# Kernel optimization log

Measured on AMD Instinct MI355X. Metric: run time of the kernel, lower is better.

## Reference

```python
import jax, jax.numpy as jnp
import numpy as np

WINDOW_SHAPE = (11, 11, 11)
CHANNELS = 1


def gaussian_nd(shape, sigma=1.0, mu=0.0):
    # n-dimensional gaussian kernel, identical to the torch source
    m = np.meshgrid(*[np.linspace(-1, 1, s) for s in shape])
    d = np.sqrt(np.sum([x * x for x in m], axis=0))
    g = np.exp(-((d - mu) ** 2 / (2.0 * sigma ** 2)))
    return g / np.sum(g)


def setup_inputs() -> dict:
    key = jax.random.key(0)
    k1, k2 = jax.random.split(key)
    shape = (2, 1, 96, 256, 256)  # N, C, D, H, W
    img1 = jax.random.uniform(k1, shape, dtype=jnp.float32)
    img2 = jax.random.uniform(k2, shape, dtype=jnp.float32)
    # depthwise window, shape (C, 1, 11, 11, 11) == (O, I/groups, D, H, W)
    w = jnp.asarray(gaussian_nd(WINDOW_SHAPE), dtype=jnp.float32)
    window = jnp.broadcast_to(w[None, None], (CHANNELS, 1) + WINDOW_SHAPE)
    return {"img1": img1, "img2": img2, "window": window}


def _blur(x, window):
    # depthwise 3D conv, padding=0 (VALID), groups=CHANNELS
    return jax.lax.conv_general_dilated(
        x, window, window_strides=(1, 1, 1), padding="VALID",
        dimension_numbers=("NCDHW", "OIDHW", "NCDHW"),
        feature_group_count=CHANNELS)


def reference(img1, img2, window):
    mu1 = _blur(img1, window)
    mu2 = _blur(img2, window)
    mu1_sq = mu1 * mu1
    mu2_sq = mu2 * mu2
    mu1_mu2 = mu1 * mu2
    sigma1_sq = _blur(img1 * img1, window) - mu1_sq
    sigma2_sq = _blur(img2 * img2, window) - mu2_sq
    sigma12 = _blur(img1 * img2, window) - mu1_mu2
    C1 = 0.01 ** 2
    C2 = 0.03 ** 2
    ssim_map = ((2 * mu1_mu2 + C1) * (2 * sigma12 + C2)
                / ((mu1_sq + mu2_sq + C1) * (sigma1_sq + sigma2_sq + C2)))
    # size_average=True -> scalar mean
    return jnp.mean(ssim_map)
```

## Files before the change

kernel.cpp:

```cpp
#include <hip/hip_runtime.h>
#include <hip/hip_fp16.h>

#define KW 11
#define NB 2
#define DI 96
#define HI 256
#define WI 256
#define DOUT 86
#define HOUT 246
#define WOUT 246
#define HT 16
#define WT 16
#define DCH 3
#define RR 26
#define HSZ (HI * WI)
#define SSIM_C1 1e-4f
#define SSIM_C2 9e-4f
#define NBLK (16 * 16 * NB * DCH)
#define RAW1_SLOT 364
#define RAW_SLOT 728

typedef const unsigned int __attribute__((address_space(1)))* gp1_t;
typedef unsigned int __attribute__((address_space(3)))* lp3_t;
using f32x2 = __attribute__((ext_vector_type(2))) float;
using f32x4 = __attribute__((ext_vector_type(4))) float;

__device__ __forceinline__ void gl_lds16(const float* g, float* l) {
    __builtin_amdgcn_global_load_lds((gp1_t)(const void*)g, (lp3_t)(void*)l, 16, 0, 0);
}

__device__ __forceinline__ f32x2 pk_fma_s(f32x2 w, f32x2 x, f32x2 acc) {
    f32x2 d;
    asm("v_pk_fma_f32 %0, %1, %2, %3" : "=v"(d) : "s"(w), "v"(x), "v"(acc));
    return d;
}

__device__ __forceinline__ unsigned pk_fma_h(unsigned w, unsigned x, unsigned acc) {
    unsigned d;
    asm("v_pk_fma_f16 %0, %1, %2, %3" : "=v"(d) : "s"(w), "v"(x), "v"(acc));
    return d;
}

__device__ __forceinline__ unsigned pkrtz(float a, float b) {
    auto h = __builtin_amdgcn_cvt_pkrtz(a, b);
    return __builtin_bit_cast(unsigned, h);
}

__device__ __forceinline__ f32x2 h2f(unsigned u) {
    f32x2 r;
    r.x = __half2float(__ushort_as_half((unsigned short)(u & 0xffffu)));
    r.y = __half2float(__ushort_as_half((unsigned short)(u >> 16)));
    return r;
}

__device__ __forceinline__ float rfl(float x) {
    return __int_as_float(__builtin_amdgcn_readfirstlane(__float_as_int(x)));
}

template<int J>
__device__ __forceinline__ void acc_step_h(
    unsigned (&AB)[KW], unsigned (&PQ)[KW], const unsigned (&wh)[KW],
    unsigned f12, unsigned f34, bool emit, unsigned& o12, unsigned& o34)
{
    #pragma unroll
    for (int p = 0; p < KW; ++p) {
        const int s = (J - p + KW) % KW;
        AB[s] = pk_fma_h(wh[p], f12, AB[s]);
        PQ[s] = pk_fma_h(wh[p], f34, PQ[s]);
    }
    const int C = (J + 1) % KW;
    if (emit) { o12 = AB[C]; o34 = PQ[C]; }
    AB[C] = 0u;
    PQ[C] = 0u;
}

static __global__ __launch_bounds__(256, 2) void ssim_main(
    const float* __restrict__ img1, const float* __restrict__ img2,
    const float* __restrict__ win, float* __restrict__ bsum)
{
    __shared__ __align__(16) float rawf[RAW_SLOT * 4];
    __shared__ __align__(16) uint2 a4h[RR][17][2];
    float* const tmpw = (float*)a4h;
    float* const w1s  = (float*)a4h + 128;
    float* const red  = (float*)a4h + 140;

    const int t = threadIdx.x;
    const int bz = blockIdx.z;
    const int n = (bz >= DCH) ? 1 : 0;
    const int chunk = bz - n * DCH;
    const int d0 = (chunk == 0) ? 0 : (chunk == 1 ? 30 : 58);
    const int dpc = (chunk == 0) ? 30 : 28;
    const int NIT = (dpc + KW - 1) >> 1;
    const int h0 = blockIdx.y * HT, w0 = blockIdx.x * WT;

    if (t < 121) {
        const int i = t / KW, j = t - i * KW;
        const float* wp = win + i * (KW * KW) + j * KW;
        float s = 0.f;
        #pragma unroll
        for (int m = 0; m < KW; ++m) s += wp[m];
        tmpw[t] = s;
    }
    __syncthreads();
    if (t < KW) {
        float s = 0.f;
        #pragma unroll
        for (int j = 0; j < KW; ++j) s += tmpw[t * KW + j];
        w1s[t] = s;
    }
    __syncthreads();
    f32x2 w2[KW];
    unsigned whq[KW];
    #pragma unroll
    for (int k = 0; k < KW; ++k) {
        const float ws = rfl(w1s[k]);
        w2[k] = (f32x2){ws, ws};
        const unsigned hb = (unsigned)__half_as_ushort(__float2half(ws));
        whq[k] = __builtin_amdgcn_readfirstlane(hb | (hb << 16));
    }
    __syncthreads();

    unsigned soff[2];
    #pragma unroll
    for (int q = 0; q < 2; ++q) {
        const int s = t + 256 * q;
        const int sl = (s >= 182) ? 1 : 0;
        const int v = (s < RAW1_SLOT ? s : 0) - sl * 182;
        const int r = v / 7;
        const int c = v - 7 * r;
        const int gh = h0 + r, gw0 = w0 + 4 * c;
        const bool oob = (s >= RAW1_SLOT) || (gh >= HI) || (gw0 >= WI);
        soff[q] = oob ? 0u
                      : (unsigned)((((n * DI + d0 + sl) * HSZ) + gh * WI + gw0) * 4);
    }
    #define STAGE() do { \
        gl_lds16((const float*)((const char*)img1 + soff[0]), &rawf[4 * t]); \
        gl_lds16((const float*)((const char*)img2 + soff[0]), &rawf[RAW1_SLOT * 4 + 4 * t]); \
        if (t < RAW1_SLOT - 256) { \
            gl_lds16((const float*)((const char*)img1 + soff[1]), &rawf[1024 + 4 * t]); \
            gl_lds16((const float*)((const char*)img2 + soff[1]), &rawf[RAW1_SLOT * 4 + 1024 + 4 * t]); \
        } \
        soff[0] += 8 * HSZ; soff[1] += 8 * HSZ; \
    } while (0)

    unsigned rABh[KW], rPQh[KW];
    #pragma unroll
    for (int p = 0; p < KW; ++p) { rABh[p] = 0u; rPQh[p] = 0u; }

    const int ty = t >> 4, tx = t & 15;
    const bool valid = (h0 + ty < HOUT) && (w0 + tx < WOUT);
    float partial = 0.f;

    const int paSl = (t >= 104) ? 1 : 0;
    const int paV  = (t < 208 ? t : 0) - paSl * 104;
    const int paCg = paV / 26;
    const int paR  = paV - paCg * 26;
    const float* const paA = &rawf[(paSl * 182 + paR * 7) * 4];
    const float* const paB = paA + RAW1_SLOT * 4;
    uint2* const paW = &a4h[paR][4 * paCg][paSl];

    auto phaseA = [&]() {
        f32x2 s12[4] = {{0.f,0.f},{0.f,0.f},{0.f,0.f},{0.f,0.f}};
        f32x2 s34[4] = {{0.f,0.f},{0.f,0.f},{0.f,0.f},{0.f,0.f}};
        #pragma unroll
        for (int q = 0; q < 4; ++q) {
            const f32x4 aq = *(const f32x4*)(paA + 4 * (paCg + q));
            const f32x4 bq = *(const f32x4*)(paB + 4 * (paCg + q));
            #pragma unroll
            for (int j = 0; j < 4; ++j) {
                const int m = 4 * q + j;
                if (m < 14) {
                    f32x2 pxy = (f32x2){aq[j], bq[j]};
                    pxy += (f32x2){-0.5f, -0.5f};
                    const float x = pxy.x, y = pxy.y;
                    const f32x2 pts = (f32x2){x * y, fmaf(x, x, y * y)};
                    #pragma unroll
                    for (int o = 0; o < 4; ++o) {
                        const int k = m - o;
                        if (k >= 0 && k <= 10) {
                            s12[o] = pk_fma_s(w2[k], pxy, s12[o]);
                            s34[o] = pk_fma_s(w2[k], pts, s34[o]);
                        }
                    }
                }
            }
        }
        #pragma unroll
        for (int o = 0; o < 4; ++o)
            paW[2 * o] = make_uint2(pkrtz(s12[o].x, s12[o].y),
                                    pkrtz(s34[o].x, s34[o].y));
    };

    STAGE();
    __syncthreads();

    int jj = 0;
    for (int i = 0; i < NIT; ++i) {
        if (t < 208) phaseA();
        __syncthreads();

        if (i + 1 < NIT) STAGE();

        unsigned ha12 = 0u, ha34 = 0u, hb12 = 0u, hb34 = 0u;
        #pragma unroll
        for (int kh = 0; kh < KW; ++kh) {
            const uint4 v = *(const uint4*)&a4h[ty + kh][tx][0];
            ha12 = pk_fma_h(whq[kh], v.x, ha12);
            ha34 = pk_fma_h(whq[kh], v.y, ha34);
            hb12 = pk_fma_h(whq[kh], v.z, hb12);
            hb34 = pk_fma_h(whq[kh], v.w, hb34);
        }

        const bool emit = (i >= 5);
        unsigned oa12u = 0u, oa34u = 0u, ob12u = 0u, ob34u = 0u;
        switch (jj) {
            #define CASE2(J) case J: \
                acc_step_h<J>(rABh, rPQh, whq, ha12, ha34, emit, oa12u, oa34u); \
                acc_step_h<(J+1)%KW>(rABh, rPQh, whq, hb12, hb34, emit, ob12u, ob34u); \
                break;
            CASE2(0) CASE2(1) CASE2(2) CASE2(3) CASE2(4) CASE2(5)
            CASE2(6) CASE2(7) CASE2(8) CASE2(9) CASE2(10)
            #undef CASE2
        }
        jj += 2; if (jj >= KW) jj -= KW;

        if (emit && valid) {
            {
                const f32x2 v12 = h2f(oa12u), v34 = h2f(oa34u);
                const float a = v12.x, b = v12.y;
                const float mu1 = a + 0.5f, mu2 = b + 0.5f;
                const float m11 = mu1 * mu1, m22 = mu2 * mu2, m12 = mu1 * mu2;
                const float s12c = v34.x - a * b;
                const float ssum = v34.y - a * a - b * b;
                const float num = (2.f * m12 + SSIM_C1) * (2.f * s12c + SSIM_C2);
                const float den = (m11 + m22 + SSIM_C1) * (ssum + SSIM_C2);
                partial += num * __builtin_amdgcn_rcpf(den);
            }
            {
                const f32x2 v12 = h2f(ob12u), v34 = h2f(ob34u);
                const float a = v12.x, b = v12.y;
                const float mu1 = a + 0.5f, mu2 = b + 0.5f;
                const float m11 = mu1 * mu1, m22 = mu2 * mu2, m12 = mu1 * mu2;
                const float s12c = v34.x - a * b;
                const float ssum = v34.y - a * a - b * b;
                const float num = (2.f * m12 + SSIM_C1) * (2.f * s12c + SSIM_C2);
                const float den = (m11 + m22 + SSIM_C1) * (ssum + SSIM_C2);
                partial += num * __builtin_amdgcn_rcpf(den);
            }
        }
        __syncthreads();
    }

    #pragma unroll
    for (int off = 32; off >= 1; off >>= 1)
        partial += __shfl_down(partial, off, 64);
    if ((t & 63) == 0) red[t >> 6] = partial;
    __syncthreads();
    if (t == 0) {
        bsum[(blockIdx.z * gridDim.y + blockIdx.y) * gridDim.x + blockIdx.x]
            = red[0] + red[1] + red[2] + red[3];
    }
}

static __global__ __launch_bounds__(256) void ssim_reduce(
    const float* __restrict__ bsum, float* __restrict__ out)
{
    __shared__ double red[4];
    const int t = threadIdx.x;
    double s = 0.0;
    for (int i = t; i < NBLK; i += 256) s += (double)bsum[i];
    #pragma unroll
    for (int off = 32; off >= 1; off >>= 1)
        s += __shfl_down(s, off, 64);
    if ((t & 63) == 0) red[t >> 6] = s;
    __syncthreads();
    if (t == 0) {
        const double tot = red[0] + red[1] + red[2] + red[3];
        out[0] = (float)(tot / (double)((long)NB * DOUT * HOUT * WOUT));
    }
}

extern "C" void kernel_launch(void* const* d_in, const int* in_sizes, int n_in,
                              void* d_out, int out_size, void* d_ws, size_t ws_size,
                              hipStream_t stream)
{
    const float* img1 = (const float*)d_in[0];
    const float* img2 = (const float*)d_in[1];
    const float* win  = (const float*)d_in[2];
    float* out  = (float*)d_out;
    float* bsum = (float*)d_ws;

    dim3 grid(16, 16, NB * DCH);
    ssim_main<<<grid, 256, 0, stream>>>(img1, img2, win, bsum);
    ssim_reduce<<<1, 256, 0, stream>>>(bsum, out);
}
```

Before: 90.28 us.

## Widen tiles to 32 columns with 512-thread blocks and four depth chunks

Doubles the output tile width to 32 and block size to 512 threads. The depth split becomes four uniform chunks of 22 slices instead of three uneven ones. The staging layout interleaves img1 and img2 per row, uses pointer strides with three load slots per thread, and expands the phase-A and reduction indexing. This cuts the horizontal halo overhead per output (the 10-column halo is spread over 32 rather than 16 columns) and changes the grid shape. In exchange, shared memory and register pressure per block grow, which may lower occupancy.

```diff
diff --git a/kernel.cpp b/kernel.cpp
--- a/kernel.cpp
+++ b/kernel.cpp
@@ -10,15 +10,18 @@
 #define HOUT 246
 #define WOUT 246
 #define HT 16
-#define WT 16
-#define DCH 3
+#define WT 32
+#define DCH 4
+#define DPC 22
 #define RR 26
 #define HSZ (HI * WI)
 #define SSIM_C1 1e-4f
 #define SSIM_C2 9e-4f
-#define NBLK (16 * 16 * NB * DCH)
-#define RAW1_SLOT 364
-#define RAW_SLOT 728
+#define NBLK (8 * 16 * NB * DCH)
+#define ROW_SLOT 23
+#define SLICE_SLOT (RR * ROW_SLOT)
+#define PAIR_SLOT (2 * SLICE_SLOT)
+#define NSTG 3
 
 typedef const unsigned int __attribute__((address_space(1)))* gp1_t;
 typedef unsigned int __attribute__((address_space(3)))* lp3_t;
@@ -74,22 +77,21 @@
     PQ[C] = 0u;
 }
 
-static __global__ __launch_bounds__(256, 2) void ssim_main(
+static __global__ __launch_bounds__(512, 2) void ssim_main(
     const float* __restrict__ img1, const float* __restrict__ img2,
     const float* __restrict__ win, float* __restrict__ bsum)
 {
-    __shared__ __align__(16) float rawf[RAW_SLOT * 4];
-    __shared__ __align__(16) uint2 a4h[RR][17][2];
+    __shared__ __align__(16) float rawf[PAIR_SLOT * 4];
+    __shared__ __align__(16) uint2 a4h[RR][33][2];
     float* const tmpw = (float*)a4h;
     float* const w1s  = (float*)a4h + 128;
-    float* const red  = (float*)a4h + 140;
+    float* const red  = (float*)a4h + 144;
 
     const int t = threadIdx.x;
     const int bz = blockIdx.z;
-    const int n = (bz >= DCH) ? 1 : 0;
-    const int chunk = bz - n * DCH;
-    const int d0 = (chunk == 0) ? 0 : (chunk == 1 ? 30 : 58);
-    const int dpc = (chunk == 0) ? 30 : 28;
+    const int n = bz >> 2, chunk = bz & 3;
+    const int d0 = chunk * DPC;
+    const int dpc = (DOUT - d0 < DPC) ? (DOUT - d0) : DPC;
     const int NIT = (dpc + KW - 1) >> 1;
     const int h0 = blockIdx.y * HT, w0 = blockIdx.x * WT;
 
@@ -120,43 +122,45 @@
     }
     __syncthreads();
 
-    unsigned soff[2];
-    #pragma unroll
-    for (int q = 0; q < 2; ++q) {
-        const int s = t + 256 * q;
-        const int sl = (s >= 182) ? 1 : 0;
-        const int v = (s < RAW1_SLOT ? s : 0) - sl * 182;
-        const int r = v / 7;
-        const int c = v - 7 * r;
+    const float* tp[NSTG];
+    int tstr[NSTG];
+    #pragma unroll
+    for (int q = 0; q < NSTG; ++q) {
+        const int u = t + 512 * q;
+        const int sl = (u >= SLICE_SLOT) ? 1 : 0;
+        const int v = (u < PAIR_SLOT ? u : 0) - sl * SLICE_SLOT;
+        const int r = v / ROW_SLOT;
+        const int rem = v - r * ROW_SLOT;
+        const int img = (rem >= 11) ? 1 : 0;
+        const int c = rem - 11 * img;
         const int gh = h0 + r, gw0 = w0 + 4 * c;
-        const bool oob = (s >= RAW1_SLOT) || (gh >= HI) || (gw0 >= WI);
-        soff[q] = oob ? 0u
-                      : (unsigned)((((n * DI + d0 + sl) * HSZ) + gh * WI + gw0) * 4);
+        const bool oob = (u >= PAIR_SLOT) || (c >= 11) || (gh >= HI) || (gw0 >= WI);
+        const float* base = img ? img2 : img1;
+        tp[q] = oob ? img1
+                    : base + ((long)(n * DI + d0 + sl) * HSZ + (long)gh * WI + gw0);
+        tstr[q] = oob ? 0 : 2 * HSZ;
     }
     #define STAGE() do { \
-        gl_lds16((const float*)((const char*)img1 + soff[0]), &rawf[4 * t]); \
-        gl_lds16((const float*)((const char*)img2 + soff[0]), &rawf[RAW1_SLOT * 4 + 4 * t]); \
-        if (t < RAW1_SLOT - 256) { \
-            gl_lds16((const float*)((const char*)img1 + soff[1]), &rawf[1024 + 4 * t]); \
-            gl_lds16((const float*)((const char*)img2 + soff[1]), &rawf[RAW1_SLOT * 4 + 1024 + 4 * t]); \
-        } \
-        soff[0] += 8 * HSZ; soff[1] += 8 * HSZ; \
+        float* db_ = &rawf[4 * t]; \
+        gl_lds16(tp[0], db_);          tp[0] += tstr[0]; \
+        gl_lds16(tp[1], db_ + 2048);   tp[1] += tstr[1]; \
+        if (t < PAIR_SLOT - 1024) { gl_lds16(tp[2], db_ + 4096); tp[2] += tstr[2]; } \
     } while (0)
 
     unsigned rABh[KW], rPQh[KW];
     #pragma unroll
     for (int p = 0; p < KW; ++p) { rABh[p] = 0u; rPQh[p] = 0u; }
 
-    const int ty = t >> 4, tx = t & 15;
+    const int ty = t >> 5, tx = t & 31;
     const bool valid = (h0 + ty < HOUT) && (w0 + tx < WOUT);
     float partial = 0.f;
 
-    const int paSl = (t >= 104) ? 1 : 0;
-    const int paV  = (t < 208 ? t : 0) - paSl * 104;
+    const int paSl = (t >= 208) ? 1 : 0;
+    const int paV  = (t < 416 ? t : 0) - paSl * 208;
     const int paCg = paV / 26;
     const int paR  = paV - paCg * 26;
-    const float* const paA = &rawf[(paSl * 182 + paR * 7) * 4];
-    const float* const paB = paA + RAW1_SLOT * 4;
+    const float* const paA = &rawf[(paSl * SLICE_SLOT + paR * ROW_SLOT) * 4];
+    const float* const paB = paA + 44;
     uint2* const paW = &a4h[paR][4 * paCg][paSl];
 
     auto phaseA = [&]() {
@@ -196,7 +200,7 @@
 
     int jj = 0;
     for (int i = 0; i < NIT; ++i) {
-        if (t < 208) phaseA();
+        if (t < 416) phaseA();
         __syncthreads();
 
         if (i + 1 < NIT) STAGE();
@@ -257,8 +261,10 @@
     if ((t & 63) == 0) red[t >> 6] = partial;
     __syncthreads();
     if (t == 0) {
-        bsum[(blockIdx.z * gridDim.y + blockIdx.y) * gridDim.x + blockIdx.x]
-            = red[0] + red[1] + red[2] + red[3];
+        float s = 0.f;
+        #pragma unroll
+        for (int wv = 0; wv < 8; ++wv) s += red[wv];
+        bsum[(blockIdx.z * gridDim.y + blockIdx.y) * gridDim.x + blockIdx.x] = s;
     }
 }
 
@@ -290,7 +296,7 @@
     float* out  = (float*)d_out;
     float* bsum = (float*)d_ws;
 
-    dim3 grid(16, 16, NB * DCH);
-    ssim_main<<<grid, 256, 0, stream>>>(img1, img2, win, bsum);
+    dim3 grid(8, 16, NB * DCH);
+    ssim_main<<<grid, 512, 0, stream>>>(img1, img2, win, bsum);
     ssim_reduce<<<1, 256, 0, stream>>>(bsum, out);
 }
```

Result: slower. 94.40 us (+4.6%).

## Double-buffer raw LDS staging with explicit vmcnt waits and fewer barriers

Applied to the files above, without the earlier changes.

Doubles the raw input LDS buffer so global-to-LDS loads run two iterations ahead, replacing __syncthreads with hand-written s_waitcnt vmcnt/s_barrier sequences tuned per wave to match the number of outstanding loads. It also drops the end-of-iteration barrier, leaving two barriers per iteration around phase A. The aim is to hide global memory latency behind compute. The larger LDS footprint may reduce occupancy, and the hand-counted vmcnt values are fragile if the compiler reorders or adds memory ops.

```diff
diff --git a/kernel.cpp b/kernel.cpp
--- a/kernel.cpp
+++ b/kernel.cpp
@@ -19,6 +19,7 @@
 #define NBLK (16 * 16 * NB * DCH)
 #define RAW1_SLOT 364
 #define RAW_SLOT 728
+#define PAIR_F (RAW_SLOT * 4)
 
 typedef const unsigned int __attribute__((address_space(1)))* gp1_t;
 typedef unsigned int __attribute__((address_space(3)))* lp3_t;
@@ -78,11 +79,11 @@
     const float* __restrict__ img1, const float* __restrict__ img2,
     const float* __restrict__ win, float* __restrict__ bsum)
 {
-    __shared__ __align__(16) float rawf[RAW_SLOT * 4];
+    __shared__ __align__(16) float rawf[2 * PAIR_F];
     __shared__ __align__(16) uint2 a4h[RR][17][2];
     float* const tmpw = (float*)a4h;
     float* const w1s  = (float*)a4h + 128;
-    float* const red  = (float*)a4h + 140;
+    float* const red  = (float*)a4h + 64;
 
     const int t = threadIdx.x;
     const int bz = blockIdx.z;
@@ -92,6 +93,7 @@
     const int dpc = (chunk == 0) ? 30 : 28;
     const int NIT = (dpc + KW - 1) >> 1;
     const int h0 = blockIdx.y * HT, w0 = blockIdx.x * WT;
+    const bool wid01 = (t >> 6) < 2;
 
     if (t < 121) {
         const int i = t / KW, j = t - i * KW;
@@ -133,12 +135,13 @@
         soff[q] = oob ? 0u
                       : (unsigned)((((n * DI + d0 + sl) * HSZ) + gh * WI + gw0) * 4);
     }
-    #define STAGE() do { \
-        gl_lds16((const float*)((const char*)img1 + soff[0]), &rawf[4 * t]); \
-        gl_lds16((const float*)((const char*)img2 + soff[0]), &rawf[RAW1_SLOT * 4 + 4 * t]); \
+    #define STAGE(pb_) do { \
+        float* db_ = &rawf[(pb_) * PAIR_F + 4 * t]; \
+        gl_lds16((const float*)((const char*)img1 + soff[0]), db_); \
+        gl_lds16((const float*)((const char*)img2 + soff[0]), db_ + RAW1_SLOT * 4); \
         if (t < RAW1_SLOT - 256) { \
-            gl_lds16((const float*)((const char*)img1 + soff[1]), &rawf[1024 + 4 * t]); \
-            gl_lds16((const float*)((const char*)img2 + soff[1]), &rawf[RAW1_SLOT * 4 + 1024 + 4 * t]); \
+            gl_lds16((const float*)((const char*)img1 + soff[1]), db_ + 1024); \
+            gl_lds16((const float*)((const char*)img2 + soff[1]), db_ + RAW1_SLOT * 4 + 1024); \
         } \
         soff[0] += 8 * HSZ; soff[1] += 8 * HSZ; \
     } while (0)
@@ -155,11 +158,11 @@
     const int paV  = (t < 208 ? t : 0) - paSl * 104;
     const int paCg = paV / 26;
     const int paR  = paV - paCg * 26;
-    const float* const paA = &rawf[(paSl * 182 + paR * 7) * 4];
-    const float* const paB = paA + RAW1_SLOT * 4;
+    const int paOff = (paSl * 182 + paR * 7) * 4;
     uint2* const paW = &a4h[paR][4 * paCg][paSl];
 
-    auto phaseA = [&]() {
+    auto phaseA = [&](const float* paA) {
+        const float* paB = paA + RAW1_SLOT * 4;
         f32x2 s12[4] = {{0.f,0.f},{0.f,0.f},{0.f,0.f},{0.f,0.f}};
         f32x2 s34[4] = {{0.f,0.f},{0.f,0.f},{0.f,0.f},{0.f,0.f}};
         #pragma unroll
@@ -191,15 +194,27 @@
                                     pkrtz(s34[o].x, s34[o].y));
     };
 
-    STAGE();
-    __syncthreads();
+    STAGE(0);
+    __builtin_amdgcn_sched_barrier(0);
+    STAGE(1);
+    __builtin_amdgcn_sched_barrier(0);
 
     int jj = 0;
     for (int i = 0; i < NIT; ++i) {
-        if (t < 208) phaseA();
-        __syncthreads();
-
-        if (i + 1 < NIT) STAGE();
+        if (i == 0 || i == NIT - 1)
+            asm volatile("s_waitcnt vmcnt(0) lgkmcnt(0)\n\ts_barrier" ::: "memory");
+        else if (wid01)
+            asm volatile("s_waitcnt vmcnt(4) lgkmcnt(0)\n\ts_barrier" ::: "memory");
+        else
+            asm volatile("s_waitcnt vmcnt(2) lgkmcnt(0)\n\ts_barrier" ::: "memory");
+        __builtin_amdgcn_sched_barrier(0);
+
+        if (t < 208) phaseA(&rawf[(i & 1) * PAIR_F + paOff]);
+
+        asm volatile("s_waitcnt lgkmcnt(0)\n\ts_barrier" ::: "memory");
+        __builtin_amdgcn_sched_barrier(0);
+
+        if (i < NIT - 2) STAGE(i & 1);
 
         unsigned ha12 = 0u, ha34 = 0u, hb12 = 0u, hb34 = 0u;
         #pragma unroll
@@ -248,12 +263,12 @@
                 partial += num * __builtin_amdgcn_rcpf(den);
             }
         }
-        __syncthreads();
     }
 
     #pragma unroll
     for (int off = 32; off >= 1; off >>= 1)
         partial += __shfl_down(partial, off, 64);
+    __syncthreads();
     if ((t & 63) == 0) red[t >> 6] = partial;
     __syncthreads();
     if (t == 0) {
```

After: 92.93 us. 1.03x slower.
